# Performance work log

Hardware: AMD Instinct MI355X
Metric: run time of the kernel (lower is better)

The kernel has to match this reference:

```python
import jax, jax.numpy as jnp
import numpy as np

# Dimensions (Llama-3-8B-style GQA with paged KV cache)
B, S, HID = 1, 1024, 4096
H, HKV, D = 32, 8, 128
G = H // HKV
BLK = 16            # tokens per KV block
NB = 256            # blocks in storage
CB = 192            # context blocks attended (3072 tokens)
PAST = 2048         # tokens already cached before this step
NL = 2              # layers in kv_ptr
L = CB * BLK


def rotate_half(x):
    x1, x2 = x[..., : x.shape[-1] // 2], x[..., x.shape[-1] // 2:]
    return jnp.concatenate([-x2, x1], axis=-1)


def setup_inputs() -> dict:
    key = jax.random.key(0)
    ks = jax.random.split(key, 8)
    hidden_states = jax.random.normal(ks[0], (B, S, HID), jnp.float32)
    kv_ptr = jax.random.normal(ks[1], (NL, 2, NB, HKV, BLK, D), jnp.float32)
    Wq = 0.02 * jax.random.normal(ks[2], (H * D, HID), jnp.float32)
    Wk = 0.02 * jax.random.normal(ks[3], (HKV * D, HID), jnp.float32)
    Wv = 0.02 * jax.random.normal(ks[4], (HKV * D, HID), jnp.float32)
    Wo = 0.02 * jax.random.normal(ks[5], (HID, H * D), jnp.float32)
    # RoPE cache for the new tokens (global positions PAST..PAST+S-1), HF convention
    pos = (PAST + jnp.arange(S)).astype(jnp.float32)
    inv_freq = 1.0 / (10000.0 ** (jnp.arange(0, D, 2, dtype=jnp.float32) / D))
    freqs = pos[:, None] * inv_freq[None, :]                # [S, D/2]
    emb = jnp.concatenate([freqs, freqs], axis=-1)           # [S, D]
    cos = jnp.cos(emb)[None, None]                           # [1,1,S,D]
    sin = jnp.sin(emb)[None, None]
    new_q_lut = jnp.arange(S, dtype=jnp.int32)[None]         # identity query LUT
    new_kv_lut = (CB - S // BLK + jnp.arange(S // BLK, dtype=jnp.int32))[None]  # blocks 128..191
    all_kv_lut = jnp.arange(CB, dtype=jnp.int32)[None]       # blocks 0..191
    kv_pos = jnp.arange(L)
    q_pos = PAST + jnp.arange(S)
    mask = (kv_pos[None, None, :] <= q_pos[None, :, None])   # [1,S,L] causal over global positions
    cmd_groups = jnp.zeros((B, S), jnp.int32)                # split-K scheduling metadata (no math effect)
    return dict(hidden_states=hidden_states, kv_ptr=kv_ptr, new_q_lut=new_q_lut,
                new_kv_lut=new_kv_lut, all_kv_lut=all_kv_lut, mask=mask,
                cmd_groups=cmd_groups, cos=cos, sin=sin, Wq=Wq, Wk=Wk, Wv=Wv, Wo=Wo,
                layer_idx=0)


def reference(hidden_states, kv_ptr, new_q_lut, new_kv_lut, all_kv_lut, mask,
              cmd_groups, cos, sin, Wq, Wk, Wv, Wo, layer_idx):
    b, s, _ = hidden_states.shape
    # QKV projections (no bias)
    q = jnp.einsum('bsh,oh->bso', hidden_states, Wq).reshape(b, s, H, D).transpose(0, 2, 1, 3)
    k = jnp.einsum('bsh,oh->bso', hidden_states, Wk).reshape(b, s, HKV, D).transpose(0, 2, 1, 3)
    v = jnp.einsum('bsh,oh->bso', hidden_states, Wv).reshape(b, s, HKV, D).transpose(0, 2, 1, 3)
    # RoPE
    q = q * cos + rotate_half(q) * sin
    k = k * cos + rotate_half(k) * sin
    # fill_kv_block_storage: scatter new K/V blocks into this layer's storage (b == 1)
    kb = jnp.transpose(k[0].reshape(HKV, s // BLK, BLK, D), (1, 0, 2, 3))  # [nblk,HKV,BLK,D]
    vb = jnp.transpose(v[0].reshape(HKV, s // BLK, BLK, D), (1, 0, 2, 3))
    sk = kv_ptr[layer_idx, 0].at[new_kv_lut[0]].set(kb)
    sv = kv_ptr[layer_idx, 1].at[new_kv_lut[0]].set(vb)
    # qkv_attention: gather context blocks via LUT, masked GQA attention
    ck = jnp.transpose(sk[all_kv_lut[0]], (1, 0, 2, 3)).reshape(HKV, L, D)  # [HKV,L,D]
    cv = jnp.transpose(sv[all_kv_lut[0]], (1, 0, 2, 3)).reshape(HKV, L, D)
    qg = q[:, :, new_q_lut[0], :].reshape(b, HKV, G, s, D)
    scores = jnp.einsum('bkgsd,kld->bkgsl', qg, ck) / jnp.sqrt(jnp.float32(D))
    scores = jnp.where(mask[:, None, None], scores, jnp.finfo(scores.dtype).min)
    p = jax.nn.softmax(scores, axis=-1)
    o = jnp.einsum('bkgsl,kld->bkgsd', p, cv).reshape(b, H, s, D)
    o = o.transpose(0, 2, 1, 3).reshape(b, s, H * D)
    return jnp.einsum('bso,ho->bsh', o, Wo)
```

## Files before the change

### kernel.cpp

```cpp
#include <hip/hip_runtime.h>
#include <cstdint>
#include <cstddef>


typedef _Float16 f16;
typedef f16 f16x8 __attribute__((ext_vector_type(8)));
typedef f16 f16x4 __attribute__((ext_vector_type(4)));
typedef float f32x4 __attribute__((ext_vector_type(4)));

#define HIDN 4096
#define LCTX 3072
#define PASTN 2048
#define QK_SCALE_LOG2 0.12753102734366334f
#define RESC_THR 11.54f

__device__ __forceinline__ f32x4 mfma16(f16x8 a, f16x8 b, f32x4 c) {
    return __builtin_amdgcn_mfma_f32_16x16x32_f16(a, b, c, 0, 0, 0);
}
__device__ __forceinline__ f32x4 mfma16k16(f16x4 a, f16x4 b, f32x4 c) {
    return __builtin_amdgcn_mfma_f32_16x16x16f16(a, b, c, 0, 0, 0);
}

__device__ __forceinline__ void gl_lds16(const void* g, void* l) {
    auto gp = (const __attribute__((address_space(1))) unsigned int*)(uintptr_t)g;
    auto lp = (__attribute__((address_space(3))) unsigned int*)(uintptr_t)l;
    __builtin_amdgcn_global_load_lds(gp, lp, 16, 0, 0);
}

__device__ __forceinline__ uint32_t lds_lo(const void* p) {
    return (uint32_t)(uintptr_t)p;
}

#define TRRD(dst, va, OFF) \
    asm volatile("ds_read_b64_tr_b16 %0, %1 offset:" #OFF : "=v"(dst) : "v"(va))
#define WAITL(N) \
    asm volatile("s_waitcnt lgkmcnt(" #N ")" ::: "memory"); \
    __builtin_amdgcn_sched_barrier(0)

__global__ void cvt_h(const float* __restrict__ hidden, f16* __restrict__ h16)
{
    int i = blockIdx.x * 256 + threadIdx.x;
    f32x4 v = *(const f32x4*)(hidden + (size_t)i * 4);
    f16x4 h;
#pragma unroll
    for (int j = 0; j < 4; j++) h[j] = (f16)v[j];
    *(f16x4*)(h16 + (size_t)i * 4) = h;
}

template <int EPI, int BM>
__global__ __launch_bounds__(256, EPI == 0 ? 2 : 3) void gemm_f16(
    const f16* __restrict__ A, const f16* __restrict__ Bh,
    const float* __restrict__ Bq, const float* __restrict__ Bk2,
    const float* __restrict__ Bv2,
    float* __restrict__ Cf, f16* __restrict__ Cq, f16* __restrict__ Ck,
    f16* __restrict__ Cv, int M, int N, int K,
    const float* __restrict__ kvp, const int* __restrict__ layer,
    f16* __restrict__ ckc, const float* __restrict__ Wo, f16* __restrict__ w16o)
{
    __shared__ f16 As[(EPI == 0 ? 2 : 1) * BM * 64];
    __shared__ f16 Bs[(EPI == 0 ? 2 : 1) * 128 * 64];

    const int bx = blockIdx.x;

    if (EPI == 0 && bx >= 384) {
        const int lay = layer[0];
        const int cid = bx - 384;
        int base = cid * 256 + threadIdx.x;
#pragma unroll
        for (int pass = 0; pass < 32; ++pass) {
            int i4 = base + pass * 32768;
            int half = i4 >> 19;
            int e = (i4 & 524287) * 4;
            int hh = e >> 18, rem = e & 262143, l = rem >> 7, d = rem & 127;
            int blk = l >> 4, rr = l & 15;
            size_t src = (((size_t)(lay * 2 + half) * 256 + blk) * 8 + hh) * 2048
                       + (size_t)rr * 128 + d;
            f32x4 x = *(const f32x4*)(kvp + src);
            f16x4 h;
#pragma unroll
            for (int j = 0; j < 4; j++) h[j] = (f16)x[j];
            size_t dst = ((size_t)hh * LCTX + l) * 128 + d;
            *(f16x4*)((half ? Cv : ckc) + dst) = h;
        }
        {
            const float* src = Wo + (size_t)cid * 131072;
            f16* dst = w16o + (size_t)cid * 131072;
#pragma unroll 4
            for (int p = 0; p < 128; ++p) {
                int e = (p * 256 + threadIdx.x) * 4;
                f32x4 v = *(const f32x4*)(src + e);
                f16x4 hv;
#pragma unroll
                for (int jx = 0; jx < 4; jx++) hv[jx] = (f16)v[jx];
                *(f16x4*)(dst + e) = hv;
            }
        }
        return;
    }

    constexpr int RPW = BM / 4;
    constexpr int MI  = BM / 32;

    const int t = threadIdx.x, lane = t & 63, w = t >> 6;
    const int wm = w >> 1, wn = w & 1;
    const int l16 = lane & 15, g16 = lane >> 4;
    const int nx = (EPI == 0) ? 48 : 32;
    const int m0 = (bx / nx) * BM, n0 = (bx % nx) * 128;

    const int srow = lane >> 3;
    const int sgr  = (lane & 7) ^ srow;

    const size_t aoff = (size_t)(m0 + w * RPW + srow) * K + sgr * 8;

    f32x4 acc[MI][4];
#pragma unroll
    for (int i = 0; i < MI; i++)
#pragma unroll
        for (int j = 0; j < 4; j++) acc[i][j] = (f32x4){0.f, 0.f, 0.f, 0.f};

    if (EPI == 0) {
        const float* Bf;
        int nb = n0;
        if (n0 >= 5120)      { Bf = Bv2; nb = n0 - 5120; }
        else if (n0 >= 4096) { Bf = Bk2; nb = n0 - 4096; }
        else                 { Bf = Bq; }
        const int brw = lane >> 4;
        const int b4  = lane & 15;
        const int bg  = b4 >> 1, bsub = (b4 & 1) << 2;
        const float* bbase = Bf + (size_t)(nb + w * 32 + brw) * K + b4 * 4;

        int bwr[8];
#pragma unroll
        for (int j = 0; j < 8; j++) {
            int r = w * 32 + j * 4 + brw;
            bwr[j] = r * 64 + ((bg ^ (r & 7)) << 3) + bsub;
        }

        f32x4 bv[8];
#pragma unroll
        for (int j = 0; j < 8; j++)
            bv[j] = *(const f32x4*)(bbase + (size_t)(j * 4) * K);
#pragma unroll
        for (int j = 0; j < 4; j++)
            gl_lds16(A + aoff + (size_t)j * 8 * K,
                     (void*)(As + (w * 32 + j * 8) * 64));
#pragma unroll
        for (int j = 0; j < 8; j++) {
            f16x4 hv;
#pragma unroll
            for (int q = 0; q < 4; q++) hv[q] = (f16)bv[j][q];
            *(f16x4*)&Bs[bwr[j]] = hv;
        }
        __syncthreads();

        for (int k0 = 0; k0 < K; k0 += 64) {
            const int cur = (k0 >> 6) & 1;
            const int nxt = cur ^ 1;
            const bool more = (k0 + 64 < K);
            if (more) {
#pragma unroll
                for (int j = 0; j < 4; j++)
                    gl_lds16(A + aoff + (size_t)j * 8 * K + k0 + 64,
                             (void*)(As + nxt * (BM * 64) + (w * 32 + j * 8) * 64));
#pragma unroll
                for (int j = 0; j < 8; j++)
                    bv[j] = *(const f32x4*)(bbase + (size_t)(j * 4) * K + k0 + 64);
            }
#pragma unroll
            for (int ks = 0; ks < 2; ks++) {
                f16x8 af[MI], bfr[4];
#pragma unroll
                for (int mi = 0; mi < MI; mi++) {
                    int r = wm * (BM / 2) + mi * 16 + l16;
                    int g = ks * 4 + g16;
                    af[mi] = *(const f16x8*)&As[cur * (BM * 64) + r * 64 + ((g ^ (r & 7)) << 3)];
                }
#pragma unroll
                for (int ni = 0; ni < 4; ni++) {
                    int r = wn * 64 + ni * 16 + l16;
                    int g = ks * 4 + g16;
                    bfr[ni] = *(const f16x8*)&Bs[cur * 8192 + r * 64 + ((g ^ (r & 7)) << 3)];
                }
#pragma unroll
                for (int ni = 0; ni < 4; ni++)
#pragma unroll
                    for (int mi = 0; mi < MI; mi++)
                        acc[mi][ni] = mfma16(af[mi], bfr[ni], acc[mi][ni]);
            }
            if (more) {
#pragma unroll
                for (int j = 0; j < 8; j++) {
                    f16x4 hv;
#pragma unroll
                    for (int q = 0; q < 4; q++) hv[q] = (f16)bv[j][q];
                    *(f16x4*)&Bs[nxt * 8192 + bwr[j]] = hv;
                }
            }
            __syncthreads();
        }
    } else {
        const size_t boff16 = (size_t)(n0 + w * 32 + srow) * K + sgr * 8;
        for (int k0 = 0; k0 < K; k0 += 64) {
#pragma unroll
            for (int j = 0; j < RPW / 8; j++)
                gl_lds16(A + aoff + (size_t)j * 8 * K + k0,
                         (void*)(As + (w * RPW + j * 8) * 64));
#pragma unroll
            for (int j = 0; j < 4; j++)
                gl_lds16(Bh + boff16 + (size_t)j * 8 * K + k0,
                         (void*)(Bs + (w * 32 + j * 8) * 64));
            __syncthreads();

#pragma unroll
            for (int ks = 0; ks < 2; ks++) {
                f16x8 af[MI], bfr[4];
#pragma unroll
                for (int mi = 0; mi < MI; mi++) {
                    int r = wm * (BM / 2) + mi * 16 + l16;
                    int g = ks * 4 + g16;
                    af[mi] = *(const f16x8*)&As[r * 64 + ((g ^ (r & 7)) << 3)];
                }
#pragma unroll
                for (int ni = 0; ni < 4; ni++) {
                    int r = wn * 64 + ni * 16 + l16;
                    int g = ks * 4 + g16;
                    bfr[ni] = *(const f16x8*)&Bs[r * 64 + ((g ^ (r & 7)) << 3)];
                }
#pragma unroll
                for (int ni = 0; ni < 4; ni++)
#pragma unroll
                    for (int mi = 0; mi < MI; mi++)
                        acc[mi][ni] = mfma16(af[mi], bfr[ni], acc[mi][ni]);
            }
            __syncthreads();
        }
    }

#pragma unroll
    for (int mi = 0; mi < MI; mi++)
#pragma unroll
        for (int ni = 0; ni < 4; ni++)
#pragma unroll
            for (int r = 0; r < 4; r++) {
                int row = m0 + wm * (BM / 2) + mi * 16 + (g16 << 2) + r;
                int col = n0 + wn * 64 + ni * 16 + l16;
                float val = acc[mi][ni][r];
                if (EPI == 0) {
                    if (col < 4096) {
                        Cq[(size_t)row * 4096 + col] = (f16)val;
                    } else if (col < 5120) {
                        Ck[(size_t)row * 1024 + (col - 4096)] = (f16)val;
                    } else {
                        int c = col - 5120;
                        int hh = c >> 7, d = c & 127;
                        Cv[((size_t)hh * LCTX + PASTN + row) * 128 + d] = (f16)val;
                    }
                } else {
                    Cf[(size_t)row * N + col] = val;
                }
            }
}

__global__ void aux2(f16* __restrict__ q16, const f16* __restrict__ kraw,
                     const float* __restrict__ cosp, const float* __restrict__ sinp,
                     f16* __restrict__ ck)
{
    int i = blockIdx.x * 256 + threadIdx.x;
    if (i < 262144) {
        int gd = i & 7, hh = (i >> 3) & 31, s = i >> 8;
        size_t b1 = (size_t)s * 4096 + hh * 128 + gd * 8;
        f16x8 x1 = *(f16x8*)(q16 + b1);
        f16x8 x2 = *(f16x8*)(q16 + b1 + 64);
        const float* c1 = cosp + s * 128 + gd * 8;
        const float* s1 = sinp + s * 128 + gd * 8;
        f16x8 o1, o2;
#pragma unroll
        for (int j = 0; j < 8; j++) {
            float a = (float)x1[j], b = (float)x2[j];
            o1[j] = (f16)((a * c1[j] - b * s1[j]) * QK_SCALE_LOG2);
            o2[j] = (f16)((b * c1[j + 64] + a * s1[j + 64]) * QK_SCALE_LOG2);
        }
        *(f16x8*)(q16 + b1) = o1;
        *(f16x8*)(q16 + b1 + 64) = o2;
    } else {
        int ii = i - 262144;
        int gd = ii & 7, kvh = (ii >> 3) & 7, s = ii >> 6;
        size_t b1 = (size_t)s * 1024 + kvh * 128 + gd * 8;
        f16x8 x1 = *(const f16x8*)(kraw + b1);
        f16x8 x2 = *(const f16x8*)(kraw + b1 + 64);
        const float* c1 = cosp + s * 128 + gd * 8;
        const float* s1 = sinp + s * 128 + gd * 8;
        f16x8 o1, o2;
#pragma unroll
        for (int j = 0; j < 8; j++) {
            float a = (float)x1[j], b = (float)x2[j];
            o1[j] = (f16)(a * c1[j] - b * s1[j]);
            o2[j] = (f16)(b * c1[j + 64] + a * s1[j + 64]);
        }
        size_t dst = ((size_t)kvh * LCTX + PASTN + s) * 128 + gd * 8;
        *(f16x8*)(ck + dst) = o1;
        *(f16x8*)(ck + dst + 64) = o2;
    }
}

__global__ __launch_bounds__(256, 2) void attn_part(
    const f16* __restrict__ Q, const f16* __restrict__ Kc,
    const f16* __restrict__ Vc, f16* __restrict__ Op, float* __restrict__ mlb)
{
    const int b = blockIdx.x;
    const int z = b >> 8;
    const int idx = b & 255;
    const int h = idx & 31;
    const int jj = idx >> 5;
    const int j = z ? (7 - jj) : jj;
    const int s0 = j * 128;
    const int kvh = h >> 2;
    const int t = threadIdx.x, lane = t & 63, w = t >> 6;
    const int l16 = lane & 15, g16 = lane >> 4;

    __shared__ f16 Ks[2][64 * 128];
    __shared__ f16 Vs[2][64 * 128];

    f16x8 qfA[4], qfB[4];
    {
        size_t baseA = (size_t)(s0 + w * 32 + l16) * 4096 + h * 128;
        size_t baseB = baseA + (size_t)16 * 4096;
#pragma unroll
        for (int kk = 0; kk < 4; kk++) {
            qfA[kk] = *(const f16x8*)(Q + baseA + kk * 32 + g16 * 8);
            qfB[kk] = *(const f16x8*)(Q + baseB + kk * 32 + g16 * 8);
        }
    }

    f32x4 ofA[8], ofB[8];
#pragma unroll
    for (int cf = 0; cf < 8; cf++) {
        ofA[cf] = (f32x4){0.f, 0.f, 0.f, 0.f};
        ofB[cf] = (f32x4){0.f, 0.f, 0.f, 0.f};
    }
    float mrA = -3.0e38f, lrA = 0.f;
    float mrB = -3.0e38f, lrB = 0.f;

    const f16* Kb = Kc + (size_t)kvh * LCTX * 128;
    const f16* Vb = Vc + (size_t)kvh * LCTX * 128;
    const int ntt = (PASTN + s0 + 128) >> 6;

    const int krow = lane >> 4;
    const int kp   = lane & 15;
    const int vrow = ((lane >> 5) << 4) + (((lane >> 3) & 3) << 2) + ((lane >> 1) & 3);
    const int vch  = (lane & 1) << 3;

    const uint32_t vs0 = lds_lo(Vs[0]) + lane * 8;
    const uint32_t vs1 = lds_lo(Vs[1]) + lane * 8;

#define STAGE_KV(l0, buf)                                                     \
    {                                                                         \
        _Pragma("unroll")                                                     \
        for (int jx = 0; jx < 4; jx++) {                                      \
            int r7 = ((jx & 1) << 2) + krow;                                  \
            int sg = kp ^ r7;                                                 \
            gl_lds16(Kb + (size_t)((l0) + w * 16 + jx * 4 + krow) * 128 + sg * 8, \
                     (void*)(Ks[buf] + (w * 16 + jx * 4) * 128));             \
        }                                                                     \
        _Pragma("unroll")                                                     \
        for (int q = 0; q < 4; q++) {                                         \
            gl_lds16(Vb + (size_t)((l0) + (q & 1) * 32 + vrow) * 128          \
                        + (w * 2 + (q >> 1)) * 16 + vch,                      \
                     (void*)(Vs[buf] + (w * 4 + q) * 512));                   \
        }                                                                     \
    }

    STAGE_KV(z * 64, 0);
    __syncthreads();

    int itp = 0;
    for (int it = z; it < ntt; it += 2, ++itp) {
        const int l0 = it << 6;
        const int cur = itp & 1;

        if (it + 2 < ntt) STAGE_KV(l0 + 128, cur ^ 1);

        f32x4 sA[4], sB[4];
#pragma unroll
        for (int ni = 0; ni < 4; ni++) {
            sA[ni] = (f32x4){0.f, 0.f, 0.f, 0.f};
            sB[ni] = (f32x4){0.f, 0.f, 0.f, 0.f};
        }
        __builtin_amdgcn_s_setprio(1);
#pragma unroll
        for (int ni = 0; ni < 4; ni++)
#pragma unroll
            for (int kk = 0; kk < 4; kk++) {
                int r = ni * 16 + l16;
                int g = kk * 4 + g16;
                f16x8 kh = *(const f16x8*)&Ks[cur][r * 128 + ((g ^ (r & 7)) << 3)];
                sA[ni] = mfma16(kh, qfA[kk], sA[ni]);
                sB[ni] = mfma16(kh, qfB[kk], sB[ni]);
            }
        __builtin_amdgcn_s_setprio(0);

#define SOFTMAX(sf, mr, lr, of, QOFF)                                          \
        {                                                                      \
            const int qrow = s0 + w * 32 + (QOFF) + l16;                       \
            if (l0 + 63 > PASTN + s0 + w * 32 + (QOFF)) {                      \
                _Pragma("unroll")                                              \
                for (int ni = 0; ni < 4; ni++)                                 \
                    _Pragma("unroll")                                          \
                    for (int r = 0; r < 4; r++) {                              \
                        int col = l0 + ni * 16 + (g16 << 2) + r;               \
                        if (col > PASTN + qrow) sf[ni][r] = -3.0e38f;          \
                    }                                                          \
            }                                                                  \
            float mx;                                                          \
            {                                                                  \
                f32x4 m4 = sf[0];                                              \
                _Pragma("unroll")                                              \
                for (int ni = 1; ni < 4; ni++) {                               \
                    m4[0] = fmaxf(m4[0], sf[ni][0]);                           \
                    m4[1] = fmaxf(m4[1], sf[ni][1]);                           \
                    m4[2] = fmaxf(m4[2], sf[ni][2]);                           \
                    m4[3] = fmaxf(m4[3], sf[ni][3]);                           \
                }                                                              \
                mx = fmaxf(fmaxf(m4[0], m4[1]), fmaxf(m4[2], m4[3]));          \
            }                                                                  \
            mx = fmaxf(mx, __shfl_xor(mx, 16));                                \
            mx = fmaxf(mx, __shfl_xor(mx, 32));                                \
            if (__any(mx > mr + RESC_THR)) {                                   \
                float mnew = fmaxf(mr, mx);                                    \
                float corr = exp2f(mr - mnew);                                 \
                mr = mnew;                                                     \
                lr *= corr;                                                    \
                float cr[4];                                                   \
                _Pragma("unroll")                                              \
                for (int r = 0; r < 4; r++) cr[r] = __shfl(corr, (g16 << 2) + r); \
                _Pragma("unroll")                                              \
                for (int cf = 0; cf < 8; cf++)                                 \
                    _Pragma("unroll")                                          \
                    for (int r = 0; r < 4; r++) of[cf][r] *= cr[r];            \
            }                                                                  \
            _Pragma("unroll")                                                  \
            for (int ni = 0; ni < 4; ni++)                                     \
                _Pragma("unroll")                                              \
                for (int r = 0; r < 4; r++) {                                  \
                    float p = exp2f(sf[ni][r] - mr);                           \
                    sf[ni][r] = p;                                             \
                    lr += p;                                                   \
                }                                                              \
        }

        SOFTMAX(sA, mrA, lrA, ofA, 0)
        SOFTMAX(sB, mrB, lrB, ofB, 16)

        f16x4 paA[4], paB[4];
#pragma unroll
        for (int ni = 0; ni < 4; ni++) {
            paA[ni][0] = (f16)sA[ni][0]; paA[ni][1] = (f16)sA[ni][1];
            paA[ni][2] = (f16)sA[ni][2]; paA[ni][3] = (f16)sA[ni][3];
            paB[ni][0] = (f16)sB[ni][0]; paB[ni][1] = (f16)sB[ni][1];
            paB[ni][2] = (f16)sB[ni][2]; paB[ni][3] = (f16)sB[ni][3];
        }

        {
            const uint32_t va = cur ? vs1 : vs0;
            f16x4 ra0, ra1, ra2, ra3, rb0, rb1, rb2, rb3;
            f16x4 rc0, rc1, rc2, rc3, rd0, rd1, rd2, rd3;
            __builtin_amdgcn_s_setprio(1);
            TRRD(ra0,va,0);     TRRD(ra1,va,512);   TRRD(ra2,va,1024);  TRRD(ra3,va,1536);
            TRRD(rb0,va,2048);  TRRD(rb1,va,2560);  TRRD(rb2,va,3072);  TRRD(rb3,va,3584);
            TRRD(rc0,va,4096);  TRRD(rc1,va,4608);  TRRD(rc2,va,5120);  TRRD(rc3,va,5632);
#define X2(cf, ni, reg) \
            ofA[cf] = mfma16k16(paA[ni], reg, ofA[cf]); \
            ofB[cf] = mfma16k16(paB[ni], reg, ofB[cf]);
            WAITL(8);
            X2(0,0,ra0) X2(0,1,ra1) X2(0,2,ra2) X2(0,3,ra3)
            TRRD(rd0,va,6144);  TRRD(rd1,va,6656);  TRRD(rd2,va,7168);  TRRD(rd3,va,7680);
            WAITL(8);
            X2(1,0,rb0) X2(1,1,rb1) X2(1,2,rb2) X2(1,3,rb3)
            TRRD(ra0,va,8192);  TRRD(ra1,va,8704);  TRRD(ra2,va,9216);  TRRD(ra3,va,9728);
            WAITL(8);
            X2(2,0,rc0) X2(2,1,rc1) X2(2,2,rc2) X2(2,3,rc3)
            TRRD(rb0,va,10240); TRRD(rb1,va,10752); TRRD(rb2,va,11264); TRRD(rb3,va,11776);
            WAITL(8);
            X2(3,0,rd0) X2(3,1,rd1) X2(3,2,rd2) X2(3,3,rd3)
            TRRD(rc0,va,12288); TRRD(rc1,va,12800); TRRD(rc2,va,13312); TRRD(rc3,va,13824);
            WAITL(8);
            X2(4,0,ra0) X2(4,1,ra1) X2(4,2,ra2) X2(4,3,ra3)
            TRRD(rd0,va,14336); TRRD(rd1,va,14848); TRRD(rd2,va,15360); TRRD(rd3,va,15872);
            WAITL(8);
            X2(5,0,rb0) X2(5,1,rb1) X2(5,2,rb2) X2(5,3,rb3)
            WAITL(4);
            X2(6,0,rc0) X2(6,1,rc1) X2(6,2,rc2) X2(6,3,rc3)
            WAITL(0);
            X2(7,0,rd0) X2(7,1,rd1) X2(7,2,rd2) X2(7,3,rd3)
#undef X2
            __builtin_amdgcn_s_setprio(0);
        }
        __syncthreads();
    }

#define WRITE_P(of, mr, lr, QOFF)                                             \
    {                                                                         \
        float l2 = lr + __shfl_xor(lr, 16);                                   \
        l2 += __shfl_xor(l2, 32);                                             \
        if (lane < 16) {                                                      \
            int srow = s0 + w * 32 + (QOFF) + lane;                           \
            *(float2*)(mlb + (((size_t)z * 1024 + srow) * 32 + h) * 2) =      \
                make_float2(mr, l2);                                          \
        }                                                                     \
        float lrr[4];                                                         \
        _Pragma("unroll")                                                     \
        for (int r = 0; r < 4; r++) lrr[r] = __shfl(l2, (g16 << 2) + r);      \
        _Pragma("unroll")                                                     \
        for (int cf = 0; cf < 8; cf++)                                        \
            _Pragma("unroll")                                                 \
            for (int r = 0; r < 4; r++) {                                     \
                int srow = s0 + w * 32 + (QOFF) + (g16 << 2) + r;             \
                int d = cf * 16 + l16;                                        \
                Op[(size_t)z * 4194304 + (size_t)srow * 4096                  \
                   + (size_t)h * 128 + d] = (f16)(of[cf][r] / lrr[r]);        \
            }                                                                 \
    }
    WRITE_P(ofA, mrA, lrA, 0)
    WRITE_P(ofB, mrB, lrB, 16)
#undef WRITE_P
#undef SOFTMAX
#undef STAGE_KV
}

__global__ void attn_combine(const f16* __restrict__ Op, const float* __restrict__ mlb,
                             f16* __restrict__ obuf)
{
    int i = blockIdx.x * 256 + threadIdx.x;
    int d8 = i & 15, hh = (i >> 4) & 31, s = i >> 9;
    float2 ml0 = *(const float2*)(mlb + (((size_t)0 * 1024 + s) * 32 + hh) * 2);
    float2 ml1 = *(const float2*)(mlb + (((size_t)1 * 1024 + s) * 32 + hh) * 2);
    float mstar = fmaxf(ml0.x, ml1.x);
    float w0 = exp2f(ml0.x - mstar) * ml0.y;
    float w1 = exp2f(ml1.x - mstar) * ml1.y;
    float inv = 1.0f / (w0 + w1);
    size_t off = (size_t)s * 4096 + (size_t)hh * 128 + d8 * 8;
    f16x8 a = *(const f16x8*)(Op + off);
    f16x8 b = *(const f16x8*)(Op + 4194304 + off);
    f16x8 o;
#pragma unroll
    for (int jx = 0; jx < 8; jx++)
        o[jx] = (f16)(((float)a[jx] * w0 + (float)b[jx] * w1) * inv);
    *(f16x8*)(obuf + off) = o;
}

extern "C" void kernel_launch(void* const* d_in, const int* in_sizes, int n_in,
                              void* d_out, int out_size, void* d_ws, size_t ws_size,
                              hipStream_t stream)
{
    const float* hidden = (const float*)d_in[0];
    const float* kvp    = (const float*)d_in[1];
    const float* cosp   = (const float*)d_in[7];
    const float* sinp   = (const float*)d_in[8];
    const float* Wq     = (const float*)d_in[9];
    const float* Wk     = (const float*)d_in[10];
    const float* Wv     = (const float*)d_in[11];
    const float* Wo     = (const float*)d_in[12];
    const int*   layer  = (const int*)d_in[13];

    char* ws = (char*)d_ws;
    f16* w16  = (f16*)ws;
    f16* opart= (f16*)(ws + 33554432);
    f16* h16  = (f16*)(ws + 50331648);
    f16* ck   = (f16*)(ws + 58720256);
    f16* cv   = (f16*)(ws + 65011712);
    f16* obuf = (f16*)(ws + 71303168);

    f16*   q16  = (f16*)d_out;
    f16*   kraw = (f16*)((char*)d_out + 8388608);
    float* mlb  = (float*)((char*)d_out + 8388608);

    cvt_h<<<4096, 256, 0, stream>>>(hidden, h16);

    gemm_f16<0, 128><<<dim3(512), 256, 0, stream>>>(
        h16, nullptr, Wq, Wk, Wv, nullptr, q16, kraw, cv, 1024, 6144, 4096,
        kvp, layer, ck, Wo, w16);

    aux2<<<1280, 256, 0, stream>>>(q16, kraw, cosp, sinp, ck);

    attn_part<<<dim3(512), 256, 0, stream>>>(q16, ck, cv, opart, mlb);

    attn_combine<<<2048, 256, 0, stream>>>(opart, mlb, obuf);

    gemm_f16<1, 64><<<dim3(512), 256, 0, stream>>>(
        obuf, w16, nullptr, nullptr, nullptr, (float*)d_out, nullptr, nullptr,
        nullptr, 1024, 4096, 4096, nullptr, nullptr, nullptr, nullptr, nullptr);
}
```

Before: 245.2 us.

## Fuse split-K attention combine into O-projection GEMM and widen QKV GEMM blocks

Removes the separate attn_combine kernel by merging the two partial attention outputs with their softmax weights while loading A tiles in the output-projection GEMM. This drops one launch and a full write/read of the combined activation buffer. The QKV GEMM is respecialised to 512-thread blocks with 8 waves, each owning a smaller sub-tile. In exchange, the fused A load loses its async global-to-LDS path and recomputes combine weights per k-tile, which adds VALU and load latency to the O-GEMM loop.

```diff
diff --git a/kernel.cpp b/kernel.cpp
--- a/kernel.cpp
+++ b/kernel.cpp
@@ -47,28 +47,28 @@
     *(f16x4*)(h16 + (size_t)i * 4) = h;
 }
 
-template <int EPI, int BM>
-__global__ __launch_bounds__(256, EPI == 0 ? 2 : 3) void gemm_f16(
-    const f16* __restrict__ A, const f16* __restrict__ Bh,
+__global__ __launch_bounds__(512, 4) void gemm_qkv(
+    const f16* __restrict__ A,
     const float* __restrict__ Bq, const float* __restrict__ Bk2,
     const float* __restrict__ Bv2,
-    float* __restrict__ Cf, f16* __restrict__ Cq, f16* __restrict__ Ck,
-    f16* __restrict__ Cv, int M, int N, int K,
+    f16* __restrict__ Cq, f16* __restrict__ Ck, f16* __restrict__ Cv,
     const float* __restrict__ kvp, const int* __restrict__ layer,
     f16* __restrict__ ckc, const float* __restrict__ Wo, f16* __restrict__ w16o)
 {
-    __shared__ f16 As[(EPI == 0 ? 2 : 1) * BM * 64];
-    __shared__ f16 Bs[(EPI == 0 ? 2 : 1) * 128 * 64];
+    constexpr int K = 4096;
+    __shared__ f16 As[2 * 128 * 64];
+    __shared__ f16 Bs[2 * 128 * 64];
 
     const int bx = blockIdx.x;
-
-    if (EPI == 0 && bx >= 384) {
+    const int t = threadIdx.x;
+
+    if (bx >= 384) {
         const int lay = layer[0];
         const int cid = bx - 384;
-        int base = cid * 256 + threadIdx.x;
-#pragma unroll
-        for (int pass = 0; pass < 32; ++pass) {
-            int i4 = base + pass * 32768;
+        int base = cid * 512 + t;
+#pragma unroll
+        for (int pass = 0; pass < 16; ++pass) {
+            int i4 = base + pass * 65536;
             int half = i4 >> 19;
             int e = (i4 & 524287) * 4;
             int hh = e >> 18, rem = e & 262143, l = rem >> 7, d = rem & 127;
@@ -86,8 +86,8 @@
             const float* src = Wo + (size_t)cid * 131072;
             f16* dst = w16o + (size_t)cid * 131072;
 #pragma unroll 4
-            for (int p = 0; p < 128; ++p) {
-                int e = (p * 256 + threadIdx.x) * 4;
+            for (int p = 0; p < 64; ++p) {
+                int e = (p * 512 + t) * 4;
                 f32x4 v = *(const f32x4*)(src + e);
                 f16x4 hv;
 #pragma unroll
@@ -98,165 +98,118 @@
         return;
     }
 
-    constexpr int RPW = BM / 4;
-    constexpr int MI  = BM / 32;
-
-    const int t = threadIdx.x, lane = t & 63, w = t >> 6;
-    const int wm = w >> 1, wn = w & 1;
+    const int lane = t & 63, w = t >> 6;
+    const int wm = w >> 2, wn = w & 3;
     const int l16 = lane & 15, g16 = lane >> 4;
-    const int nx = (EPI == 0) ? 48 : 32;
-    const int m0 = (bx / nx) * BM, n0 = (bx % nx) * 128;
+    const int m0 = (bx / 48) * 128, n0 = (bx % 48) * 128;
 
     const int srow = lane >> 3;
     const int sgr  = (lane & 7) ^ srow;
-
-    const size_t aoff = (size_t)(m0 + w * RPW + srow) * K + sgr * 8;
-
-    f32x4 acc[MI][4];
-#pragma unroll
-    for (int i = 0; i < MI; i++)
-#pragma unroll
-        for (int j = 0; j < 4; j++) acc[i][j] = (f32x4){0.f, 0.f, 0.f, 0.f};
-
-    if (EPI == 0) {
-        const float* Bf;
-        int nb = n0;
-        if (n0 >= 5120)      { Bf = Bv2; nb = n0 - 5120; }
-        else if (n0 >= 4096) { Bf = Bk2; nb = n0 - 4096; }
-        else                 { Bf = Bq; }
-        const int brw = lane >> 4;
-        const int b4  = lane & 15;
-        const int bg  = b4 >> 1, bsub = (b4 & 1) << 2;
-        const float* bbase = Bf + (size_t)(nb + w * 32 + brw) * K + b4 * 4;
-
-        int bwr[8];
-#pragma unroll
-        for (int j = 0; j < 8; j++) {
-            int r = w * 32 + j * 4 + brw;
-            bwr[j] = r * 64 + ((bg ^ (r & 7)) << 3) + bsub;
-        }
-
-        f32x4 bv[8];
-#pragma unroll
-        for (int j = 0; j < 8; j++)
-            bv[j] = *(const f32x4*)(bbase + (size_t)(j * 4) * K);
-#pragma unroll
-        for (int j = 0; j < 4; j++)
-            gl_lds16(A + aoff + (size_t)j * 8 * K,
-                     (void*)(As + (w * 32 + j * 8) * 64));
-#pragma unroll
-        for (int j = 0; j < 8; j++) {
-            f16x4 hv;
-#pragma unroll
-            for (int q = 0; q < 4; q++) hv[q] = (f16)bv[j][q];
-            *(f16x4*)&Bs[bwr[j]] = hv;
+    const size_t aoff = (size_t)(m0 + w * 16 + srow) * K + sgr * 8;
+
+    const float* Bf;
+    int nb = n0;
+    if (n0 >= 5120)      { Bf = Bv2; nb = n0 - 5120; }
+    else if (n0 >= 4096) { Bf = Bk2; nb = n0 - 4096; }
+    else                 { Bf = Bq; }
+    const int brw = lane >> 4;
+    const int b4  = lane & 15;
+    const int bg  = b4 >> 1, bsub = (b4 & 1) << 2;
+    const float* bbase = Bf + (size_t)(nb + w * 16 + brw) * K + b4 * 4;
+
+    int bwr[4];
+#pragma unroll
+    for (int j = 0; j < 4; j++) {
+        int r = w * 16 + j * 4 + brw;
+        bwr[j] = r * 64 + ((bg ^ (r & 7)) << 3) + bsub;
+    }
+
+    f32x4 acc[4][2];
+#pragma unroll
+    for (int i = 0; i < 4; i++)
+#pragma unroll
+        for (int j = 0; j < 2; j++) acc[i][j] = (f32x4){0.f, 0.f, 0.f, 0.f};
+
+    f32x4 bv[4];
+#pragma unroll
+    for (int j = 0; j < 4; j++)
+        bv[j] = *(const f32x4*)(bbase + (size_t)(j * 4) * K);
+#pragma unroll
+    for (int j = 0; j < 2; j++)
+        gl_lds16(A + aoff + (size_t)j * 8 * K,
+                 (void*)(As + (w * 16 + j * 8) * 64));
+#pragma unroll
+    for (int j = 0; j < 4; j++) {
+        f16x4 hv;
+#pragma unroll
+        for (int q = 0; q < 4; q++) hv[q] = (f16)bv[j][q];
+        *(f16x4*)&Bs[bwr[j]] = hv;
+    }
+    __syncthreads();
+
+    for (int k0 = 0; k0 < K; k0 += 64) {
+        const int cur = (k0 >> 6) & 1;
+        const int nxt = cur ^ 1;
+        const bool more = (k0 + 64 < K);
+        if (more) {
+#pragma unroll
+            for (int j = 0; j < 2; j++)
+                gl_lds16(A + aoff + (size_t)j * 8 * K + k0 + 64,
+                         (void*)(As + nxt * 8192 + (w * 16 + j * 8) * 64));
+#pragma unroll
+            for (int j = 0; j < 4; j++)
+                bv[j] = *(const f32x4*)(bbase + (size_t)(j * 4) * K + k0 + 64);
+        }
+#pragma unroll
+        for (int ks = 0; ks < 2; ks++) {
+            f16x8 af[4], bfr[2];
+#pragma unroll
+            for (int mi = 0; mi < 4; mi++) {
+                int r = wm * 64 + mi * 16 + l16;
+                int g = ks * 4 + g16;
+                af[mi] = *(const f16x8*)&As[cur * 8192 + r * 64 + ((g ^ (r & 7)) << 3)];
+            }
+#pragma unroll
+            for (int ni = 0; ni < 2; ni++) {
+                int r = wn * 32 + ni * 16 + l16;
+                int g = ks * 4 + g16;
+                bfr[ni] = *(const f16x8*)&Bs[cur * 8192 + r * 64 + ((g ^ (r & 7)) << 3)];
+            }
+#pragma unroll
+            for (int ni = 0; ni < 2; ni++)
+#pragma unroll
+                for (int mi = 0; mi < 4; mi++)
+                    acc[mi][ni] = mfma16(af[mi], bfr[ni], acc[mi][ni]);
+        }
+        if (more) {
+#pragma unroll
+            for (int j = 0; j < 4; j++) {
+                f16x4 hv;
+#pragma unroll
+                for (int q = 0; q < 4; q++) hv[q] = (f16)bv[j][q];
+                *(f16x4*)&Bs[nxt * 8192 + bwr[j]] = hv;
+            }
         }
         __syncthreads();
-
-        for (int k0 = 0; k0 < K; k0 += 64) {
-            const int cur = (k0 >> 6) & 1;
-            const int nxt = cur ^ 1;
-            const bool more = (k0 + 64 < K);
-            if (more) {
-#pragma unroll
-                for (int j = 0; j < 4; j++)
-                    gl_lds16(A + aoff + (size_t)j * 8 * K + k0 + 64,
-                             (void*)(As + nxt * (BM * 64) + (w * 32 + j * 8) * 64));
-#pragma unroll
-                for (int j = 0; j < 8; j++)
-                    bv[j] = *(const f32x4*)(bbase + (size_t)(j * 4) * K + k0 + 64);
-            }
-#pragma unroll
-            for (int ks = 0; ks < 2; ks++) {
-                f16x8 af[MI], bfr[4];
-#pragma unroll
-                for (int mi = 0; mi < MI; mi++) {
-                    int r = wm * (BM / 2) + mi * 16 + l16;
-                    int g = ks * 4 + g16;
-                    af[mi] = *(const f16x8*)&As[cur * (BM * 64) + r * 64 + ((g ^ (r & 7)) << 3)];
-                }
-#pragma unroll
-                for (int ni = 0; ni < 4; ni++) {
-                    int r = wn * 64 + ni * 16 + l16;
-                    int g = ks * 4 + g16;
-                    bfr[ni] = *(const f16x8*)&Bs[cur * 8192 + r * 64 + ((g ^ (r & 7)) << 3)];
-                }
-#pragma unroll
-                for (int ni = 0; ni < 4; ni++)
-#pragma unroll
-                    for (int mi = 0; mi < MI; mi++)
-                        acc[mi][ni] = mfma16(af[mi], bfr[ni], acc[mi][ni]);
-            }
-            if (more) {
-#pragma unroll
-                for (int j = 0; j < 8; j++) {
-                    f16x4 hv;
-#pragma unroll
-                    for (int q = 0; q < 4; q++) hv[q] = (f16)bv[j][q];
-                    *(f16x4*)&Bs[nxt * 8192 + bwr[j]] = hv;
-                }
-            }
-            __syncthreads();
-        }
-    } else {
-        const size_t boff16 = (size_t)(n0 + w * 32 + srow) * K + sgr * 8;
-        for (int k0 = 0; k0 < K; k0 += 64) {
-#pragma unroll
-            for (int j = 0; j < RPW / 8; j++)
-                gl_lds16(A + aoff + (size_t)j * 8 * K + k0,
-                         (void*)(As + (w * RPW + j * 8) * 64));
-#pragma unroll
-            for (int j = 0; j < 4; j++)
-                gl_lds16(Bh + boff16 + (size_t)j * 8 * K + k0,
-                         (void*)(Bs + (w * 32 + j * 8) * 64));
-            __syncthreads();
-
-#pragma unroll
-            for (int ks = 0; ks < 2; ks++) {
-                f16x8 af[MI], bfr[4];
-#pragma unroll
-                for (int mi = 0; mi < MI; mi++) {
-                    int r = wm * (BM / 2) + mi * 16 + l16;
-                    int g = ks * 4 + g16;
-                    af[mi] = *(const f16x8*)&As[r * 64 + ((g ^ (r & 7)) << 3)];
-                }
-#pragma unroll
-                for (int ni = 0; ni < 4; ni++) {
-                    int r = wn * 64 + ni * 16 + l16;
-                    int g = ks * 4 + g16;
-                    bfr[ni] = *(const f16x8*)&Bs[r * 64 + ((g ^ (r & 7)) << 3)];
-                }
-#pragma unroll
-                for (int ni = 0; ni < 4; ni++)
-#pragma unroll
-                    for (int mi = 0; mi < MI; mi++)
-                        acc[mi][ni] = mfma16(af[mi], bfr[ni], acc[mi][ni]);
-            }
-            __syncthreads();
-        }
-    }
-
-#pragma unroll
-    for (int mi = 0; mi < MI; mi++)
-#pragma unroll
-        for (int ni = 0; ni < 4; ni++)
+    }
+
+#pragma unroll
+    for (int mi = 0; mi < 4; mi++)
+#pragma unroll
+        for (int ni = 0; ni < 2; ni++)
 #pragma unroll
             for (int r = 0; r < 4; r++) {
-                int row = m0 + wm * (BM / 2) + mi * 16 + (g16 << 2) + r;
-                int col = n0 + wn * 64 + ni * 16 + l16;
+                int row = m0 + wm * 64 + mi * 16 + (g16 << 2) + r;
+                int col = n0 + wn * 32 + ni * 16 + l16;
                 float val = acc[mi][ni][r];
-                if (EPI == 0) {
-                    if (col < 4096) {
-                        Cq[(size_t)row * 4096 + col] = (f16)val;
-                    } else if (col < 5120) {
-                        Ck[(size_t)row * 1024 + (col - 4096)] = (f16)val;
-                    } else {
-                        int c = col - 5120;
-                        int hh = c >> 7, d = c & 127;
-                        Cv[((size_t)hh * LCTX + PASTN + row) * 128 + d] = (f16)val;
-                    }
+                if (col < 4096) {
+                    Cq[(size_t)row * 4096 + col] = (f16)val;
+                } else if (col < 5120) {
+                    Ck[(size_t)row * 1024 + (col - 4096)] = (f16)val;
                 } else {
-                    Cf[(size_t)row * N + col] = val;
+                    int c = col - 5120;
+                    int hh = c >> 7, d = c & 127;
+                    Cv[((size_t)hh * LCTX + PASTN + row) * 128 + d] = (f16)val;
                 }
             }
 }
@@ -527,25 +480,94 @@
 #undef STAGE_KV
 }
 
-__global__ void attn_combine(const f16* __restrict__ Op, const float* __restrict__ mlb,
-                             f16* __restrict__ obuf)
+__global__ __launch_bounds__(256, 3) void gemm_o(
+    const f16* __restrict__ Op, const float* __restrict__ mlb,
+    const f16* __restrict__ Bh, float* __restrict__ Cf)
 {
-    int i = blockIdx.x * 256 + threadIdx.x;
-    int d8 = i & 15, hh = (i >> 4) & 31, s = i >> 9;
-    float2 ml0 = *(const float2*)(mlb + (((size_t)0 * 1024 + s) * 32 + hh) * 2);
-    float2 ml1 = *(const float2*)(mlb + (((size_t)1 * 1024 + s) * 32 + hh) * 2);
-    float mstar = fmaxf(ml0.x, ml1.x);
-    float w0 = exp2f(ml0.x - mstar) * ml0.y;
-    float w1 = exp2f(ml1.x - mstar) * ml1.y;
-    float inv = 1.0f / (w0 + w1);
-    size_t off = (size_t)s * 4096 + (size_t)hh * 128 + d8 * 8;
-    f16x8 a = *(const f16x8*)(Op + off);
-    f16x8 b = *(const f16x8*)(Op + 4194304 + off);
-    f16x8 o;
-#pragma unroll
-    for (int jx = 0; jx < 8; jx++)
-        o[jx] = (f16)(((float)a[jx] * w0 + (float)b[jx] * w1) * inv);
-    *(f16x8*)(obuf + off) = o;
+    constexpr int K = 4096;
+    __shared__ f16 As[64 * 64];
+    __shared__ f16 Bs[128 * 64];
+
+    const int bx = blockIdx.x;
+    const int t = threadIdx.x, lane = t & 63, w = t >> 6;
+    const int wm = w >> 1, wn = w & 1;
+    const int l16 = lane & 15, g16 = lane >> 4;
+    const int m0 = (bx / 32) * 64, n0 = (bx % 32) * 128;
+
+    const int srow = lane >> 3;
+    const int sgr  = (lane & 7) ^ srow;
+
+    const size_t boff16 = (size_t)(n0 + w * 32 + srow) * K + sgr * 8;
+
+    f32x4 acc[2][4];
+#pragma unroll
+    for (int i = 0; i < 2; i++)
+#pragma unroll
+        for (int j = 0; j < 4; j++) acc[i][j] = (f32x4){0.f, 0.f, 0.f, 0.f};
+
+    for (int k0 = 0; k0 < K; k0 += 64) {
+        {
+            const int hh = k0 >> 7;
+#pragma unroll
+            for (int j = 0; j < 2; j++) {
+                int row = m0 + w * 16 + j * 8 + srow;
+                int col = k0 + sgr * 8;
+                float2 ml0 = *(const float2*)(mlb + (((size_t)row) * 32 + hh) * 2);
+                float2 ml1 = *(const float2*)(mlb + (((size_t)1024 + row) * 32 + hh) * 2);
+                float mstar = fmaxf(ml0.x, ml1.x);
+                float w0 = exp2f(ml0.x - mstar) * ml0.y;
+                float w1 = exp2f(ml1.x - mstar) * ml1.y;
+                float inv = 1.0f / (w0 + w1);
+                w0 *= inv; w1 *= inv;
+                f16x8 a0 = *(const f16x8*)(Op + (size_t)row * 4096 + col);
+                f16x8 a1 = *(const f16x8*)(Op + 4194304 + (size_t)row * 4096 + col);
+                f16x8 av;
+#pragma unroll
+                for (int q = 0; q < 8; q++)
+                    av[q] = (f16)((float)a0[q] * w0 + (float)a1[q] * w1);
+                *(f16x8*)&As[(w * 16 + j * 8) * 64 + lane * 8] = av;
+            }
+        }
+#pragma unroll
+        for (int j = 0; j < 4; j++)
+            gl_lds16(Bh + boff16 + (size_t)j * 8 * K + k0,
+                     (void*)(Bs + (w * 32 + j * 8) * 64));
+        __syncthreads();
+
+#pragma unroll
+        for (int ks = 0; ks < 2; ks++) {
+            f16x8 af[2], bfr[4];
+#pragma unroll
+            for (int mi = 0; mi < 2; mi++) {
+                int r = wm * 32 + mi * 16 + l16;
+                int g = ks * 4 + g16;
+                af[mi] = *(const f16x8*)&As[r * 64 + ((g ^ (r & 7)) << 3)];
+            }
+#pragma unroll
+            for (int ni = 0; ni < 4; ni++) {
+                int r = wn * 64 + ni * 16 + l16;
+                int g = ks * 4 + g16;
+                bfr[ni] = *(const f16x8*)&Bs[r * 64 + ((g ^ (r & 7)) << 3)];
+            }
+#pragma unroll
+            for (int ni = 0; ni < 4; ni++)
+#pragma unroll
+                for (int mi = 0; mi < 2; mi++)
+                    acc[mi][ni] = mfma16(af[mi], bfr[ni], acc[mi][ni]);
+        }
+        __syncthreads();
+    }
+
+#pragma unroll
+    for (int mi = 0; mi < 2; mi++)
+#pragma unroll
+        for (int ni = 0; ni < 4; ni++)
+#pragma unroll
+            for (int r = 0; r < 4; r++) {
+                int row = m0 + wm * 32 + mi * 16 + (g16 << 2) + r;
+                int col = n0 + wn * 64 + ni * 16 + l16;
+                Cf[(size_t)row * 4096 + col] = acc[mi][ni][r];
+            }
 }
 
 extern "C" void kernel_launch(void* const* d_in, const int* in_sizes, int n_in,
@@ -563,30 +585,24 @@
     const int*   layer  = (const int*)d_in[13];
 
     char* ws = (char*)d_ws;
-    f16* w16  = (f16*)ws;
-    f16* opart= (f16*)(ws + 33554432);
-    f16* h16  = (f16*)(ws + 50331648);
-    f16* ck   = (f16*)(ws + 58720256);
-    f16* cv   = (f16*)(ws + 65011712);
-    f16* obuf = (f16*)(ws + 71303168);
-
-    f16*   q16  = (f16*)d_out;
-    f16*   kraw = (f16*)((char*)d_out + 8388608);
-    float* mlb  = (float*)((char*)d_out + 8388608);
+    f16*   w16  = (f16*)ws;
+    f16*   opart= (f16*)(ws + 33554432);
+    f16*   h16  = (f16*)(ws + 50331648);
+    f16*   ck   = (f16*)(ws + 58720256);
+    f16*   cv   = (f16*)(ws + 65011712);
+    float* mlb  = (float*)(ws + 71303168);
+
+    f16* q16  = (f16*)d_out;
+    f16* kraw = (f16*)((char*)d_out + 8388608);
 
     cvt_h<<<4096, 256, 0, stream>>>(hidden, h16);
 
-    gemm_f16<0, 128><<<dim3(512), 256, 0, stream>>>(
-        h16, nullptr, Wq, Wk, Wv, nullptr, q16, kraw, cv, 1024, 6144, 4096,
-        kvp, layer, ck, Wo, w16);
+    gemm_qkv<<<dim3(512), 512, 0, stream>>>(
+        h16, Wq, Wk, Wv, q16, kraw, cv, kvp, layer, ck, Wo, w16);
 
     aux2<<<1280, 256, 0, stream>>>(q16, kraw, cosp, sinp, ck);
 
     attn_part<<<dim3(512), 256, 0, stream>>>(q16, ck, cv, opart, mlb);
 
-    attn_combine<<<2048, 256, 0, stream>>>(opart, mlb, obuf);
-
-    gemm_f16<1, 64><<<dim3(512), 256, 0, stream>>>(
-        obuf, w16, nullptr, nullptr, nullptr, (float*)d_out, nullptr, nullptr,
-        nullptr, 1024, 4096, 4096, nullptr, nullptr, nullptr, nullptr, nullptr);
-}
+    gemm_o<<<dim3(512), 256, 0, stream>>>(opart, mlb, w16, (float*)d_out);
+}
```

Result: slower. 276.4 us (+12.7%).
